# Optimization experiments

Measured on AMD Instinct MI355X. Metric: run time of the kernel, lower is better.

## Reference

```python
import jax, jax.numpy as jnp
import numpy as np

N = 1024   # number of points (pairwise stage is N x N)
D = 16     # input_dim
H = 32     # hidden_dim
O = 3      # out_dim


def setup_inputs() -> dict:
    key = jax.random.key(0)
    ks = jax.random.split(key, 16)
    p = lambda k, shape: jax.random.normal(k, shape, jnp.float32) * 0.1
    return {
        'x': jax.random.normal(ks[0], (N, D), jnp.float32),
        'proj1_w': p(ks[1], (H, 2 * D)), 'proj1_b': p(ks[2], (H,)),
        'gru1_wih': p(ks[3], (3 * H, H)), 'gru1_whh': p(ks[4], (3 * H, H)),
        'gru1_bih': p(ks[5], (3 * H,)), 'gru1_bhh': p(ks[6], (3 * H,)),
        'proj2_w': p(ks[7], (H, 2 * H)), 'proj2_b': p(ks[8], (H,)),
        'gru2_wih': p(ks[9], (3 * H, H)), 'gru2_whh': p(ks[10], (3 * H, H)),
        'gru2_bih': p(ks[11], (3 * H,)), 'gru2_bhh': p(ks[12], (3 * H,)),
        'clf_w': p(ks[13], (O, H)), 'clf_b': p(ks[14], (O,)),
    }


def _pairwise_relu(feat, w, b):
    # feat: [N, F] -> relu(Linear(cat([f_i, f_j - f_i]))): [N, N, H]
    n, f = feat.shape
    fi = jnp.broadcast_to(feat[:, None, :], (n, n, f))
    fj = jnp.broadcast_to(feat[None, :, :], (n, n, f))
    diffs = jnp.concatenate([fi, fj - fi], axis=-1)  # [N, N, 2F]
    return jax.nn.relu(jnp.einsum('ijf,hf->ijh', diffs, w) + b)


def _gru_last(seq, wih, whh, bih, bhh):
    # seq: [B, T, H_in] (batch_first). Returns final hidden state [B, H].
    # PyTorch GRU gate order: r, z, n.
    xg = jnp.einsum('bti,gi->tbg', seq, wih) + bih  # precompute input gates [T,B,3H]
    h_dim = whh.shape[1]

    def step(h, g):
        xr, xz, xn = jnp.split(g, 3, axis=-1)
        hr, hz, hn = jnp.split(h @ whh.T + bhh, 3, axis=-1)
        r = jax.nn.sigmoid(xr + hr)
        z = jax.nn.sigmoid(xz + hz)
        n = jnp.tanh(xn + r * hn)
        return (1.0 - z) * n + z * h, None

    h0 = jnp.zeros((seq.shape[0], h_dim), seq.dtype)
    h_last, _ = jax.lax.scan(step, h0, xg)
    return h_last


def reference(x, proj1_w, proj1_b, gru1_wih, gru1_whh, gru1_bih, gru1_bhh,
              proj2_w, proj2_b, gru2_wih, gru2_whh, gru2_bih, gru2_bhh,
              clf_w, clf_b):
    out1 = _pairwise_relu(x, proj1_w, proj1_b)            # [N, N, H]
    h1 = _gru_last(out1, gru1_wih, gru1_whh, gru1_bih, gru1_bhh)  # [N, H]
    out2 = _pairwise_relu(h1, proj2_w, proj2_b)           # [N, N, H]
    h2 = _gru_last(out2, gru2_wih, gru2_whh, gru2_bih, gru2_bhh)  # [N, H]
    return h2 @ clf_w.T + clf_b                           # [N, O]
```

## Files before the change

kernel.cpp:

```cpp
#include <hip/hip_runtime.h>


typedef _Float16 hv2 __attribute__((ext_vector_type(2)));
typedef _Float16 hv8 __attribute__((ext_vector_type(8)));
typedef float    fv4 __attribute__((ext_vector_type(4)));
typedef unsigned uv4 __attribute__((ext_vector_type(4)));

__device__ __forceinline__ unsigned pkh(float a, float b) {
    auto t = __builtin_amdgcn_cvt_pkrtz(a, b);
    return __builtin_bit_cast(unsigned, t);
}
__device__ __forceinline__ fv4 splat4(float v) { return fv4{v, v, v, v}; }
#if __has_builtin(__builtin_amdgcn_rcpf)
__device__ __forceinline__ float frcp(float x) { return __builtin_amdgcn_rcpf(x); }
#else
__device__ __forceinline__ float frcp(float x) { return 1.f / x; }
#endif
#if __has_builtin(__builtin_amdgcn_fdot2)
__device__ __forceinline__ float d2(unsigned a, unsigned b, float c) {
    return __builtin_amdgcn_fdot2(__builtin_bit_cast(hv2, a),
                                  __builtin_bit_cast(hv2, b), c, false);
}
#else
__device__ __forceinline__ float d2(unsigned a, unsigned b, float c) {
    hv2 x = __builtin_bit_cast(hv2, a), y = __builtin_bit_cast(hv2, b);
    return fmaf((float)x.x, (float)y.x, fmaf((float)x.y, (float)y.y, c));
}
#endif
__device__ __forceinline__ float dpp_xor1(float x) {
    int r = __builtin_amdgcn_update_dpp(0, __builtin_bit_cast(int, x),
                                        0xB1, 0xF, 0xF, true);
    return __builtin_bit_cast(float, r);
}
__device__ __forceinline__ void half_swap(float x, float& lo_all, float& hi_all) {
    float d = x, s = x;
    asm("v_permlane32_swap_b32 %0, %1" : "+v"(d), "+v"(s));
    lo_all = d;
    hi_all = s;
}

__global__ void proj1_kernel(const float* __restrict__ x, const float* __restrict__ w,
                             const float* __restrict__ bias,
                             float* __restrict__ A, float* __restrict__ B) {
    int idx = blockIdx.x * 256 + threadIdx.x;
    int i = idx >> 5, h = idx & 31;
    float sa = bias[h];
    float sb = 0.f;
#pragma unroll
    for (int d = 0; d < 16; ++d) {
        float xv = x[i * 16 + d];
        float wa = w[h * 32 + d];
        float wb = w[h * 32 + 16 + d];
        sa += (wa - wb) * xv;
        sb += wb * xv;
    }
    A[i * 32 + h] = sa;
    B[i * 32 + h] = sb;
}

__global__ void proj2_kernel(const float* __restrict__ h1, const float* __restrict__ w,
                             const float* __restrict__ bias,
                             float* __restrict__ A, float* __restrict__ B) {
    int idx = blockIdx.x * 256 + threadIdx.x;
    int i = idx >> 5, h = idx & 31;
    float sa = bias[h];
    float sb = 0.f;
#pragma unroll
    for (int k = 0; k < 32; ++k) {
        float hv = h1[i * 32 + k];
        float wa = w[h * 64 + k];
        float wb = w[h * 64 + 32 + k];
        sa += (wa - wb) * hv;
        sb += wb * hv;
    }
    A[i * 32 + h] = sa;
    B[i * 32 + h] = sb;
}

__global__ __launch_bounds__(64, 1) void gru_kernel(
    const float* __restrict__ A, const float* __restrict__ B,
    const float* __restrict__ wih, const float* __restrict__ whh,
    const float* __restrict__ bih, const float* __restrict__ bhh,
    float* __restrict__ h_out) {
    const int l = threadIdx.x;
    const int q = l >> 4;
    const int m0 = l & 15;
    const int m = l & 31;
    const int c = blockIdx.x;

    __shared__ float xg[6][16][17];

    hv8 WI[6];
#pragma unroll
    for (int T = 0; T < 6; ++T) {
        int g = 16 * T + m0;
        uv4 wi;
#pragma unroll
        for (int r = 0; r < 4; ++r) {
            int lo = 4 * q + r;
            wi[r] = pkh(wih[g * 32 + lo], wih[g * 32 + lo + 16]);
        }
        WI[T] = __builtin_bit_cast(hv8, wi);
    }
    float bi[6];
#pragma unroll
    for (int T = 0; T < 6; ++T) bi[T] = bih[16 * T + m0];

    const int grow = (l < 32) ? m : (32 + m);
    unsigned grz[16], wn2[16];
#pragma unroll
    for (int k = 0; k < 16; ++k) {
        grz[k] = pkh(whh[grow * 32 + 2 * k],     whh[grow * 32 + 2 * k + 1]);
        wn2[k] = pkh(whh[(64 + m) * 32 + 2 * k], whh[(64 + m) * 32 + 2 * k + 1]);
    }
    const float brz = bhh[grow];
    const float bhn = bhh[64 + m];

    const fv4* A4 = (const fv4*)A;
    const fv4* B4 = (const fv4*)B;
    const fv4 alo = A4[c * 8 + q];
    const fv4 ahi = A4[c * 8 + 4 + q];

    fv4 blo = B4[m0 * 8 + q], bhi = B4[m0 * 8 + 4 + q];

    float h_l = 0.f;

    for (int c0 = 0; c0 < 1024; c0 += 16) {
        uv4 xb;
#pragma unroll
        for (int r = 0; r < 4; ++r)
            xb[r] = pkh(fmaxf(alo[r] + blo[r], 0.f), fmaxf(ahi[r] + bhi[r], 0.f));
        hv8 xf = __builtin_bit_cast(hv8, xb);

        int nc = (c0 + 16) & 1023;
        blo = B4[(nc + m0) * 8 + q];
        bhi = B4[(nc + m0) * 8 + 4 + q];

#pragma unroll
        for (int T = 0; T < 6; ++T) {
            fv4 D = __builtin_amdgcn_mfma_f32_16x16x32_f16(xf, WI[T], splat4(bi[T]), 0, 0, 0);
            if (T < 4) {
#pragma unroll
                for (int r = 0; r < 4; ++r) xg[T][4 * q + r][m0] = __expf(-D[r]);
            } else {
#pragma unroll
                for (int r = 0; r < 4; ++r) xg[T][4 * q + r][m0] = D[r];
            }
        }
        __syncthreads();

        const int Tq = m >> 4;
        const int mc = m & 15;
        float er = xg[Tq][0][mc];
        float ez = xg[2 + Tq][0][mc];
        float xn = xg[4 + Tq][0][mc];

#pragma unroll
        for (int it = 0; it < 16; ++it) {
            float hnb = dpp_xor1(h_l);
            hv2 hp;
            hp.x = (_Float16)h_l;
            hp.y = (_Float16)hnb;
            unsigned pk = __builtin_bit_cast(unsigned, hp);
            unsigned Hs[16];
#pragma unroll
            for (int k = 0; k < 16; ++k)
                Hs[k] = (unsigned)__builtin_amdgcn_readlane((int)pk, 2 * k);

            float ga = brz, gb = 0.f, gc = 0.f, gd = 0.f;
#pragma unroll
            for (int k = 0; k < 4; ++k) {
                ga = d2(grz[k],      Hs[k],      ga);
                gb = d2(grz[k + 4],  Hs[k + 4],  gb);
                gc = d2(grz[k + 8],  Hs[k + 8],  gc);
                gd = d2(grz[k + 12], Hs[k + 12], gd);
            }
            float gfull = (ga + gb) + (gc + gd);
            float hr, hz;
            half_swap(gfull, hr, hz);

            float ehr = __expf(-hr);
            float ehz = __expf(-hz);

            float na = bhn, nb2 = 0.f, nc2 = 0.f, nd2 = 0.f;
#pragma unroll
            for (int k = 0; k < 4; ++k) {
                na  = d2(wn2[k],      Hs[k],      na);
                nb2 = d2(wn2[k + 4],  Hs[k + 4],  nb2);
                nc2 = d2(wn2[k + 8],  Hs[k + 8],  nc2);
                nd2 = d2(wn2[k + 12], Hs[k + 12], nd2);
            }
            float hn = (na + nb2) + (nc2 + nd2);

            int nt = (it + 1) & 15;
            float ner = xg[Tq][nt][mc];
            float nez = xg[2 + Tq][nt][mc];
            float nxn = xg[4 + Tq][nt][mc];

            float r = frcp(fmaf(er, ehr, 1.f));
            float z = frcp(fmaf(ez, ehz, 1.f));
            float n = 1.f - 2.f * frcp(__expf(2.f * (xn + r * hn)) + 1.f);
            h_l = (1.f - z) * n + z * h_l;

            er = ner; ez = nez; xn = nxn;
        }
        __syncthreads();
    }

    if (l < 32) h_out[c * 32 + m] = h_l;
}

__global__ void clf_kernel(const float* __restrict__ h2v, const float* __restrict__ w,
                           const float* __restrict__ bias, float* __restrict__ out) {
    int idx = blockIdx.x * 256 + threadIdx.x;
    if (idx >= 3072) return;
    int i = idx / 3, o = idx - i * 3;
    float s = bias[o];
#pragma unroll
    for (int k = 0; k < 32; ++k) s += w[o * 32 + k] * h2v[i * 32 + k];
    out[idx] = s;
}

extern "C" void kernel_launch(void* const* d_in, const int* in_sizes, int n_in,
                              void* d_out, int out_size, void* d_ws, size_t ws_size,
                              hipStream_t stream) {
    const float* x       = (const float*)d_in[0];
    const float* p1w     = (const float*)d_in[1];
    const float* p1b     = (const float*)d_in[2];
    const float* g1_wih  = (const float*)d_in[3];
    const float* g1_whh  = (const float*)d_in[4];
    const float* g1_bih  = (const float*)d_in[5];
    const float* g1_bhh  = (const float*)d_in[6];
    const float* p2w     = (const float*)d_in[7];
    const float* p2b     = (const float*)d_in[8];
    const float* g2_wih  = (const float*)d_in[9];
    const float* g2_whh  = (const float*)d_in[10];
    const float* g2_bih  = (const float*)d_in[11];
    const float* g2_bhh  = (const float*)d_in[12];
    const float* clfw    = (const float*)d_in[13];
    const float* clfb    = (const float*)d_in[14];

    float* ws = (float*)d_ws;
    float* A  = ws;
    float* Bt = ws + 32768;
    float* h  = ws + 65536;

    proj1_kernel<<<128, 256, 0, stream>>>(x, p1w, p1b, A, Bt);
    gru_kernel<<<1024, 64, 0, stream>>>(A, Bt, g1_wih, g1_whh, g1_bih, g1_bhh, h);
    proj2_kernel<<<128, 256, 0, stream>>>(h, p2w, p2b, A, Bt);
    gru_kernel<<<1024, 64, 0, stream>>>(A, Bt, g2_wih, g2_whh, g2_bih, g2_bhh, h);
    clf_kernel<<<12, 256, 0, stream>>>(h, clfw, clfb, (float*)d_out);
}
```

Before: 497.0 us.

## Fold exp2 scaling into GRU weights, vectorize gate LDS, fuse classifier

Pre-scales the input and hidden GRU weights and biases by -log2(e) and 2*log2(e), so the recurrent step uses raw exp2 with no extra multiplies. The serial update is reassociated to shorten the dependency chain per timestep. Gate values are now stored and read from LDS as float4 in a transposed, padded layout and consumed four steps at a time. The classifier is fused into the tail of the second GRU launch, which removes one kernel launch. Folding the scales into the weights before fp16 packing slightly changes rounding.

```diff
diff --git a/kernel.cpp b/kernel.cpp
--- a/kernel.cpp
+++ b/kernel.cpp
@@ -16,6 +16,11 @@
 #else
 __device__ __forceinline__ float frcp(float x) { return 1.f / x; }
 #endif
+#if __has_builtin(__builtin_amdgcn_exp2f)
+__device__ __forceinline__ float fexp2(float x) { return __builtin_amdgcn_exp2f(x); }
+#else
+__device__ __forceinline__ float fexp2(float x) { return exp2f(x); }
+#endif
 #if __has_builtin(__builtin_amdgcn_fdot2)
 __device__ __forceinline__ float d2(unsigned a, unsigned b, float c) {
     return __builtin_amdgcn_fdot2(__builtin_bit_cast(hv2, a),
@@ -38,6 +43,9 @@
     lo_all = d;
     hi_all = s;
 }
+
+#define SRZ (-1.44269504088896341f)
+#define SN  ( 2.88539008177792682f)
 
 __global__ void proj1_kernel(const float* __restrict__ x, const float* __restrict__ w,
                              const float* __restrict__ bias,
@@ -81,40 +89,43 @@
     const float* __restrict__ A, const float* __restrict__ B,
     const float* __restrict__ wih, const float* __restrict__ whh,
     const float* __restrict__ bih, const float* __restrict__ bhh,
-    float* __restrict__ h_out) {
+    float* __restrict__ h_out,
+    const float* __restrict__ clfw, const float* __restrict__ clfb,
+    float* __restrict__ out3) {
     const int l = threadIdx.x;
     const int q = l >> 4;
     const int m0 = l & 15;
     const int m = l & 31;
     const int c = blockIdx.x;
 
-    __shared__ float xg[6][16][17];
+    __shared__ float xg[6][16][20];
 
     hv8 WI[6];
 #pragma unroll
     for (int T = 0; T < 6; ++T) {
+        const float sc = (T < 4) ? SRZ : SN;
         int g = 16 * T + m0;
         uv4 wi;
 #pragma unroll
         for (int r = 0; r < 4; ++r) {
             int lo = 4 * q + r;
-            wi[r] = pkh(wih[g * 32 + lo], wih[g * 32 + lo + 16]);
+            wi[r] = pkh(wih[g * 32 + lo] * sc, wih[g * 32 + lo + 16] * sc);
         }
         WI[T] = __builtin_bit_cast(hv8, wi);
     }
     float bi[6];
 #pragma unroll
-    for (int T = 0; T < 6; ++T) bi[T] = bih[16 * T + m0];
+    for (int T = 0; T < 6; ++T) bi[T] = bih[16 * T + m0] * ((T < 4) ? SRZ : SN);
 
     const int grow = (l < 32) ? m : (32 + m);
     unsigned grz[16], wn2[16];
 #pragma unroll
     for (int k = 0; k < 16; ++k) {
-        grz[k] = pkh(whh[grow * 32 + 2 * k],     whh[grow * 32 + 2 * k + 1]);
-        wn2[k] = pkh(whh[(64 + m) * 32 + 2 * k], whh[(64 + m) * 32 + 2 * k + 1]);
-    }
-    const float brz = bhh[grow];
-    const float bhn = bhh[64 + m];
+        grz[k] = pkh(whh[grow * 32 + 2 * k] * SRZ,     whh[grow * 32 + 2 * k + 1] * SRZ);
+        wn2[k] = pkh(whh[(64 + m) * 32 + 2 * k] * SN,  whh[(64 + m) * 32 + 2 * k + 1] * SN);
+    }
+    const float brz  = bhh[grow] * SRZ;
+    const float bhn2 = bhh[64 + m] * SN;
 
     const fv4* A4 = (const fv4*)A;
     const fv4* B4 = (const fv4*)B;
@@ -125,6 +136,9 @@
 
     float h_l = 0.f;
 
+    const int Tq = m >> 4;
+    const int mc = m & 15;
+
     for (int c0 = 0; c0 < 1024; c0 += 16) {
         uv4 xb;
 #pragma unroll
@@ -139,86 +153,99 @@
 #pragma unroll
         for (int T = 0; T < 6; ++T) {
             fv4 D = __builtin_amdgcn_mfma_f32_16x16x32_f16(xf, WI[T], splat4(bi[T]), 0, 0, 0);
+            fv4 e;
             if (T < 4) {
 #pragma unroll
-                for (int r = 0; r < 4; ++r) xg[T][4 * q + r][m0] = __expf(-D[r]);
+                for (int r = 0; r < 4; ++r) e[r] = fexp2(D[r]);
             } else {
-#pragma unroll
-                for (int r = 0; r < 4; ++r) xg[T][4 * q + r][m0] = D[r];
+                e = D;
             }
+            *(fv4*)&xg[T][m0][4 * q] = e;
         }
         __syncthreads();
 
-        const int Tq = m >> 4;
-        const int mc = m & 15;
-        float er = xg[Tq][0][mc];
-        float ez = xg[2 + Tq][0][mc];
-        float xn = xg[4 + Tq][0][mc];
-
-#pragma unroll
-        for (int it = 0; it < 16; ++it) {
-            float hnb = dpp_xor1(h_l);
-            hv2 hp;
-            hp.x = (_Float16)h_l;
-            hp.y = (_Float16)hnb;
-            unsigned pk = __builtin_bit_cast(unsigned, hp);
-            unsigned Hs[16];
-#pragma unroll
-            for (int k = 0; k < 16; ++k)
-                Hs[k] = (unsigned)__builtin_amdgcn_readlane((int)pk, 2 * k);
-
-            float ga = brz, gb = 0.f, gc = 0.f, gd = 0.f;
-#pragma unroll
-            for (int k = 0; k < 4; ++k) {
-                ga = d2(grz[k],      Hs[k],      ga);
-                gb = d2(grz[k + 4],  Hs[k + 4],  gb);
-                gc = d2(grz[k + 8],  Hs[k + 8],  gc);
-                gd = d2(grz[k + 12], Hs[k + 12], gd);
+        fv4 Er = *(const fv4*)&xg[Tq][mc][0];
+        fv4 Ez = *(const fv4*)&xg[2 + Tq][mc][0];
+        fv4 Xn = *(const fv4*)&xg[4 + Tq][mc][0];
+
+#pragma unroll
+        for (int g = 0; g < 4; ++g) {
+            const fv4 cEr = Er, cEz = Ez, cXn = Xn;
+            int ng = (g + 1) & 3;
+            Er = *(const fv4*)&xg[Tq][mc][4 * ng];
+            Ez = *(const fv4*)&xg[2 + Tq][mc][4 * ng];
+            Xn = *(const fv4*)&xg[4 + Tq][mc][4 * ng];
+
+#pragma unroll
+            for (int j = 0; j < 4; ++j) {
+                const float er = cEr[j];
+                const float ez = cEz[j];
+                const float xn = cXn[j];
+
+                float hnb = dpp_xor1(h_l);
+                hv2 hp;
+                hp.x = (_Float16)h_l;
+                hp.y = (_Float16)hnb;
+                unsigned pk = __builtin_bit_cast(unsigned, hp);
+                unsigned Hs[16];
+#pragma unroll
+                for (int k = 0; k < 16; ++k)
+                    Hs[k] = (unsigned)__builtin_amdgcn_readlane((int)pk, 2 * k);
+
+                float ga = brz, gb = 0.f, gc = 0.f, gd = 0.f;
+#pragma unroll
+                for (int k = 0; k < 4; ++k) {
+                    ga = d2(grz[k],      Hs[k],      ga);
+                    gb = d2(grz[k + 4],  Hs[k + 4],  gb);
+                    gc = d2(grz[k + 8],  Hs[k + 8],  gc);
+                    gd = d2(grz[k + 12], Hs[k + 12], gd);
+                }
+                float gfull = (ga + gb) + (gc + gd);
+                float hrs, hzs;
+                half_swap(gfull, hrs, hzs);
+
+                float ehr = fexp2(hrs);
+                float ehz = fexp2(hzs);
+
+                float na = bhn2, nb2 = 0.f, nc2 = 0.f, nd2 = 0.f;
+#pragma unroll
+                for (int k = 0; k < 4; ++k) {
+                    na  = d2(wn2[k],      Hs[k],      na);
+                    nb2 = d2(wn2[k + 4],  Hs[k + 4],  nb2);
+                    nc2 = d2(wn2[k + 8],  Hs[k + 8],  nc2);
+                    nd2 = d2(wn2[k + 12], Hs[k + 12], nd2);
+                }
+                float hn2 = (na + nb2) + (nc2 + nd2);
+
+                float z   = frcp(fmaf(ez, ehz, 1.f));
+                float zh  = z * h_l;
+                float omz = 1.f - z;
+                float s   = zh + omz;
+                float t2  = -2.f * omz;
+
+                float r  = frcp(fmaf(er, ehr, 1.f));
+                float y  = fmaf(r, hn2, xn);
+                float E  = fexp2(y);
+                float rE = frcp(E + 1.f);
+                h_l = fmaf(t2, rE, s);
             }
-            float gfull = (ga + gb) + (gc + gd);
-            float hr, hz;
-            half_swap(gfull, hr, hz);
-
-            float ehr = __expf(-hr);
-            float ehz = __expf(-hz);
-
-            float na = bhn, nb2 = 0.f, nc2 = 0.f, nd2 = 0.f;
-#pragma unroll
-            for (int k = 0; k < 4; ++k) {
-                na  = d2(wn2[k],      Hs[k],      na);
-                nb2 = d2(wn2[k + 4],  Hs[k + 4],  nb2);
-                nc2 = d2(wn2[k + 8],  Hs[k + 8],  nc2);
-                nd2 = d2(wn2[k + 12], Hs[k + 12], nd2);
-            }
-            float hn = (na + nb2) + (nc2 + nd2);
-
-            int nt = (it + 1) & 15;
-            float ner = xg[Tq][nt][mc];
-            float nez = xg[2 + Tq][nt][mc];
-            float nxn = xg[4 + Tq][nt][mc];
-
-            float r = frcp(fmaf(er, ehr, 1.f));
-            float z = frcp(fmaf(ez, ehz, 1.f));
-            float n = 1.f - 2.f * frcp(__expf(2.f * (xn + r * hn)) + 1.f);
-            h_l = (1.f - z) * n + z * h_l;
-
-            er = ner; ez = nez; xn = nxn;
         }
         __syncthreads();
     }
 
-    if (l < 32) h_out[c * 32 + m] = h_l;
-}
-
-__global__ void clf_kernel(const float* __restrict__ h2v, const float* __restrict__ w,
-                           const float* __restrict__ bias, float* __restrict__ out) {
-    int idx = blockIdx.x * 256 + threadIdx.x;
-    if (idx >= 3072) return;
-    int i = idx / 3, o = idx - i * 3;
-    float s = bias[o];
-#pragma unroll
-    for (int k = 0; k < 32; ++k) s += w[o * 32 + k] * h2v[i * 32 + k];
-    out[idx] = s;
+    if (clfw) {
+        float* hs = (float*)xg;
+        if (l < 32) hs[m] = h_l;
+        __syncthreads();
+        if (l < 3) {
+            float s = clfb[l];
+#pragma unroll
+            for (int k = 0; k < 32; ++k) s += clfw[l * 32 + k] * hs[k];
+            out3[c * 3 + l] = s;
+        }
+    } else {
+        if (l < 32) h_out[c * 32 + m] = h_l;
+    }
 }
 
 extern "C" void kernel_launch(void* const* d_in, const int* in_sizes, int n_in,
@@ -246,8 +273,9 @@
     float* h  = ws + 65536;
 
     proj1_kernel<<<128, 256, 0, stream>>>(x, p1w, p1b, A, Bt);
-    gru_kernel<<<1024, 64, 0, stream>>>(A, Bt, g1_wih, g1_whh, g1_bih, g1_bhh, h);
+    gru_kernel<<<1024, 64, 0, stream>>>(A, Bt, g1_wih, g1_whh, g1_bih, g1_bhh, h,
+                                        nullptr, nullptr, nullptr);
     proj2_kernel<<<128, 256, 0, stream>>>(h, p2w, p2b, A, Bt);
-    gru_kernel<<<1024, 64, 0, stream>>>(A, Bt, g2_wih, g2_whh, g2_bih, g2_bhh, h);
-    clf_kernel<<<12, 256, 0, stream>>>(h, clfw, clfb, (float*)d_out);
-}
+    gru_kernel<<<1024, 64, 0, stream>>>(A, Bt, g2_wih, g2_whh, g2_bih, g2_bhh, h,
+                                        clfw, clfb, (float*)d_out);
+}
```

After: 456.1 us. -8.2%, faster.
